# Optimization experiments

Measured on AMD Instinct MI355X. Metric: run time of the kernel, lower is better.

## Reference

```python
import jax, jax.numpy as jnp
import numpy as np
import math

HIDDEN_DIM = 1024
NUM_HEADS = 16
HEAD_DIM = HIDDEN_DIM // NUM_HEADS  # 64

def setup_inputs() -> dict:
    key = jax.random.key(0)
    k1, k2, k3 = jax.random.split(key, 3)
    x = jax.random.normal(k1, (8, 4096, HIDDEN_DIM), dtype=jnp.float32)
    W = jax.random.normal(k2, (HIDDEN_DIM, NUM_HEADS), dtype=jnp.float32) * (1.0 / math.sqrt(HIDDEN_DIM))
    mask = jax.random.randint(k3, (8, 4096), 0, 2, dtype=jnp.int32)
    return {"x": x, "W": W, "mask": mask}

def reference(x, W, mask):
    B, S, D = x.shape
    # linear scoring: [B,S,H], scaled by sqrt(head_dim)
    logits = jnp.einsum('bsd,dh->bsh', x, W) / math.sqrt(HEAD_DIM)
    # mask out padded positions (mask==0 -> -inf) before softmax over seq axis
    logits = jnp.where(mask[:, :, None] == 0, -jnp.inf, logits)
    attn = jax.nn.softmax(logits, axis=1)  # softmax over sequence dim
    # dropout is identity in eval mode
    # weighted sum: original expands x over heads, so each head pools the full hidden vector
    pooled = jnp.einsum('bsh,bsd->bhd', attn, x)  # [B, H, D]
    return pooled.reshape(B, NUM_HEADS * D)
```

## Files before the change

### kernel.cpp

```cpp
#include <hip/hip_runtime.h>
#include <math.h>

#define BB 8
#define SS 4096
#define DD 1024
#define HH 16

typedef __attribute__((ext_vector_type(4))) float f32x4;
typedef __fp16 fp16x2 __attribute__((ext_vector_type(2)));
typedef _Float16 half8v __attribute__((ext_vector_type(8)));


__device__ __forceinline__ void sm_merge(float& m, float& z, float om, float oz) {
  float nm = fmaxf(m, om);
  if (nm > -INFINITY)
    z = z * __expf(m - nm) + oz * __expf(om - nm);
  m = nm;
}

__global__ __launch_bounds__(256) void k_prepw(
    const float* __restrict__ W, ushort* __restrict__ wh16, ushort* __restrict__ wl16) {
  int i = blockIdx.x * 256 + threadIdx.x;
  int t = i >> 9;
  int l = (i >> 3) & 63;
  int e = i & 7;
  int d = t * 32 + (l >> 4) * 8 + e;
  int h = l & 15;
  float w = W[d * HH + h];
  _Float16 wh = (_Float16)w;
  _Float16 wl = (_Float16)(w - (float)wh);
  union { _Float16 f; ushort u; } ch, cl;
  ch.f = wh; cl.f = wl;
  wh16[i] = ch.u;
  wl16[i] = cl.u;
}

#define XLOAD(dst, c)                                                          \
  _Pragma("unroll") for (int k = 0; k < 4; ++k) {                              \
    int row = k * 4 + srow;                                                    \
    dst[k] = *reinterpret_cast<const float4*>(                                 \
        xw + (size_t)row * DD + (c) * 64 + sul * 4);                           \
  }
#define XSTAGE(src, c)                                                         \
  _Pragma("unroll") for (int k = 0; k < 4; ++k) {                              \
    int row = k * 4 + srow;                                                    \
    lds4[(c) & 1][wv][row][sul ^ (row & 7)] = src[k];                          \
  }
#define WLOAD(c)                                                               \
  whf[(c) & 1][0] = bhp[(2 * (c) + 0) * 64];                                   \
  whf[(c) & 1][1] = bhp[(2 * (c) + 1) * 64];                                   \
  wlf[(c) & 1][0] = blp[(2 * (c) + 0) * 64];                                   \
  wlf[(c) & 1][1] = blp[(2 * (c) + 1) * 64];

__global__ __launch_bounds__(256, 2) void k_logits(
    const float* __restrict__ x, const ushort* __restrict__ wh16,
    const ushort* __restrict__ wl16, const int* __restrict__ mask,
    float* __restrict__ plog, float2* __restrict__ bred) {
  __shared__ float4 lds4[2][4][16][16];
  __shared__ float2 smch[4][16];

  const int tid = threadIdx.x;
  const int lane = tid & 63;
  const int wv = __builtin_amdgcn_readfirstlane(tid >> 6);
  const int b = blockIdx.x >> 6;
  const int tile = blockIdx.x & 63;
  const int s0 = tile * 64;
  const int r15 = lane & 15;
  const int kg = lane >> 4;
  const int srow = lane >> 4;
  const int sul = lane & 15;

  const float* xw = x + ((size_t)b * SS + s0 + wv * 16) * DD;
  const half8v* bhp = reinterpret_cast<const half8v*>(wh16) + lane;
  const half8v* blp = reinterpret_cast<const half8v*>(wl16) + lane;

  f32x4 acch = {0.f, 0.f, 0.f, 0.f};
  f32x4 accl = {0.f, 0.f, 0.f, 0.f};
  float4 st[3][4];
  half8v whf[2][2], wlf[2][2];

  XLOAD(st[0], 0);
  XLOAD(st[1], 1);
  XLOAD(st[2], 2);
  XSTAGE(st[0], 0);
  WLOAD(0);
  WLOAD(1);

#pragma unroll
  for (int c = 0; c < 16; ++c) {
    if (c < 13) { XLOAD(st[(c + 3) % 3], c + 3); }

#pragma unroll
    for (int t4 = 0; t4 < 2; ++t4) {
      const int u0 = t4 * 8 + kg * 2;
      float4 va = lds4[c & 1][wv][r15][u0 ^ (r15 & 7)];
      float4 vb = lds4[c & 1][wv][r15][(u0 + 1) ^ (r15 & 7)];
      union { fp16x2 h2[4]; half8v h8; } ax;
      ax.h2[0] = __builtin_amdgcn_cvt_pkrtz(va.x, va.y);
      ax.h2[1] = __builtin_amdgcn_cvt_pkrtz(va.z, va.w);
      ax.h2[2] = __builtin_amdgcn_cvt_pkrtz(vb.x, vb.y);
      ax.h2[3] = __builtin_amdgcn_cvt_pkrtz(vb.z, vb.w);
      acch = __builtin_amdgcn_mfma_f32_16x16x32_f16(ax.h8, whf[c & 1][t4], acch, 0, 0, 0);
      accl = __builtin_amdgcn_mfma_f32_16x16x32_f16(ax.h8, wlf[c & 1][t4], accl, 0, 0, 0);
    }

    if (c < 14) { WLOAD(c + 2); }
    if (c < 15) { XSTAGE(st[(c + 1) % 3], c + 1); }
  }

  float lv[4];
  float* ob = plog + ((size_t)b * SS + s0 + wv * 16) * HH;
#pragma unroll
  for (int q = 0; q < 4; ++q) {
    int srw = kg * 4 + q;
    int msk = mask[b * SS + s0 + wv * 16 + srw];
    float v = (acch[q] + accl[q]) * 0.125f;
    lv[q] = msk ? v : -INFINITY;
    ob[(size_t)srw * HH + r15] = lv[q];
  }
  float ml = fmaxf(fmaxf(lv[0], lv[1]), fmaxf(lv[2], lv[3]));
  float zl = 0.f;
  if (ml > -INFINITY) {
#pragma unroll
    for (int q = 0; q < 4; ++q) zl += __expf(lv[q] - ml);
  }
#pragma unroll
  for (int off = 16; off < 64; off <<= 1) {
    float om = __shfl_xor(ml, off, 64);
    float oz = __shfl_xor(zl, off, 64);
    sm_merge(ml, zl, om, oz);
  }
  if (kg == 0) smch[wv][r15] = make_float2(ml, zl);
  __syncthreads();
  if (tid < 16) {
    float2 p0 = smch[0][tid];
    float m = p0.x, z = p0.y;
#pragma unroll
    for (int w = 1; w < 4; ++w) {
      float2 pw = smch[w][tid];
      sm_merge(m, z, pw.x, pw.y);
    }
    bred[((size_t)b * 64 + tile) * HH + tid] = make_float2(m, z);
  }
}

__global__ __launch_bounds__(256) void k_pool(
    const float* __restrict__ x, const float* __restrict__ plog,
    const float2* __restrict__ bred, const int* __restrict__ mask,
    float* __restrict__ partial) {
  __shared__ float wl[128][16];
  __shared__ float fm[16], fz[16];
  const int tid = threadIdx.x;
  const int dh = blockIdx.x & 1;
  const int sc = (blockIdx.x >> 1) & 31;
  const int b = blockIdx.x >> 6;
  const int s0 = sc * 128;

  if (tid < 16) {
    float m = -INFINITY, z = 0.f;
#pragma unroll 4
    for (int c = 0; c < 64; ++c) {
      float2 p = bred[((size_t)b * 64 + c) * HH + tid];
      sm_merge(m, z, p.x, p.y);
    }
    fm[tid] = m;
    fz[tid] = (z > 0.f) ? 1.0f / z : 0.f;
  }
  __syncthreads();

  const float4* p0 = reinterpret_cast<const float4*>(plog + ((size_t)b * SS + s0) * HH);
  const int* mb = mask + b * SS + s0;
#pragma unroll
  for (int k = 0; k < 2; ++k) {
    int f = k * 256 + tid;
    float4 va = p0[f];
    int msk = mb[f >> 2];
    int hb = (f & 3) * 4;
    float4 w;
    w.x = msk ? __expf(va.x - fm[hb + 0]) * fz[hb + 0] : 0.f;
    w.y = msk ? __expf(va.y - fm[hb + 1]) * fz[hb + 1] : 0.f;
    w.z = msk ? __expf(va.z - fm[hb + 2]) * fz[hb + 2] : 0.f;
    w.w = msk ? __expf(va.w - fm[hb + 3]) * fz[hb + 3] : 0.f;
    *reinterpret_cast<float4*>(&wl[0][0] + f * 4) = w;
  }
  __syncthreads();

  float2 acc[HH];
#pragma unroll
  for (int h = 0; h < HH; ++h) acc[h] = make_float2(0.f, 0.f);

  const float* xb = x + ((size_t)b * SS + s0) * DD + dh * 512 + tid * 2;
  for (int s = 0; s < 128; ++s) {
    float2 xv = *reinterpret_cast<const float2*>(xb + (size_t)s * DD);
    const float4* wrow = reinterpret_cast<const float4*>(wl[s]);
    float4 wa = wrow[0], wb_ = wrow[1], wc = wrow[2], wd = wrow[3];
    float wvv[16] = {wa.x, wa.y, wa.z, wa.w, wb_.x, wb_.y, wb_.z, wb_.w,
                     wc.x, wc.y, wc.z, wc.w, wd.x, wd.y, wd.z, wd.w};
#pragma unroll
    for (int h = 0; h < HH; ++h) {
      float w = wvv[h];
      acc[h].x += w * xv.x;
      acc[h].y += w * xv.y;
    }
  }

  float* pb = partial + ((size_t)sc * BB + b) * (HH * DD) + dh * 512 + tid * 2;
#pragma unroll
  for (int h = 0; h < HH; ++h)
    *reinterpret_cast<float2*>(pb + (size_t)h * DD) = acc[h];
}

__global__ __launch_bounds__(256) void k_reduce(
    const float* __restrict__ partial, float* __restrict__ out) {
  const int idx = blockIdx.x * 256 + threadIdx.x;
  float s = 0.f;
#pragma unroll
  for (int c = 0; c < 32; ++c) s += partial[(size_t)c * (BB * HH * DD) + idx];
  out[idx] = s;
}

extern "C" void kernel_launch(void* const* d_in, const int* in_sizes, int n_in,
                              void* d_out, int out_size, void* d_ws, size_t ws_size,
                              hipStream_t stream) {
  const float* x = (const float*)d_in[0];
  const float* W = (const float*)d_in[1];
  const int* mask = (const int*)d_in[2];
  float* out = (float*)d_out;

  char* ws = (char*)d_ws;
  float* plog    = (float*)ws;
  float* partial = (float*)(ws + (size_t)6 * 1024 * 1024);
  ushort* wh16   = (ushort*)(ws + (size_t)22 * 1024 * 1024);
  ushort* wl16   = (ushort*)(ws + (size_t)22 * 1024 * 1024 + 32 * 1024);
  float2* bred   = (float2*)(ws + (size_t)23 * 1024 * 1024);

  k_prepw<<<64, 256, 0, stream>>>(W, wh16, wl16);
  k_logits<<<512, 256, 0, stream>>>(x, wh16, wl16, mask, plog, bred);
  k_pool<<<512, 256, 0, stream>>>(x, plog, bred, mask, partial);
  k_reduce<<<512, 256, 0, stream>>>(partial, out);
}
```

Measured before the change: 70.99 us.

## Drop split-fp16 weight correction and pool from fp16 copy of x

Removes the low-part fp16 weight term, so logits are computed with a single fp16 MFMA instead of a hi/lo pair. The logits kernel also writes an fp16 copy of x into workspace, and the pooling kernel reads that copy instead of fp32 x. This halves the bytes the second pass over x reads, at the cost of an extra fp16 write. It lowers accuracy for both the logits and the pooled output, which may break tolerance.

After: 84.13 us. +18.5%, slower.

```diff
diff --git a/kernel.cpp b/kernel.cpp
--- a/kernel.cpp
+++ b/kernel.cpp
@@ -19,20 +19,16 @@
 }
 
 __global__ __launch_bounds__(256) void k_prepw(
-    const float* __restrict__ W, ushort* __restrict__ wh16, ushort* __restrict__ wl16) {
+    const float* __restrict__ W, ushort* __restrict__ wh16) {
   int i = blockIdx.x * 256 + threadIdx.x;
   int t = i >> 9;
   int l = (i >> 3) & 63;
   int e = i & 7;
   int d = t * 32 + (l >> 4) * 8 + e;
   int h = l & 15;
-  float w = W[d * HH + h];
-  _Float16 wh = (_Float16)w;
-  _Float16 wl = (_Float16)(w - (float)wh);
-  union { _Float16 f; ushort u; } ch, cl;
-  ch.f = wh; cl.f = wl;
-  wh16[i] = ch.u;
-  wl16[i] = cl.u;
+  union { _Float16 f; ushort u; } cv;
+  cv.f = (_Float16)W[d * HH + h];
+  wh16[i] = cv.u;
 }
 
 #define XLOAD(dst, c)                                                          \
@@ -48,14 +44,12 @@
   }
 #define WLOAD(c)                                                               \
   whf[(c) & 1][0] = bhp[(2 * (c) + 0) * 64];                                   \
-  whf[(c) & 1][1] = bhp[(2 * (c) + 1) * 64];                                   \
-  wlf[(c) & 1][0] = blp[(2 * (c) + 0) * 64];                                   \
-  wlf[(c) & 1][1] = blp[(2 * (c) + 1) * 64];
+  whf[(c) & 1][1] = bhp[(2 * (c) + 1) * 64];
 
 __global__ __launch_bounds__(256, 2) void k_logits(
     const float* __restrict__ x, const ushort* __restrict__ wh16,
-    const ushort* __restrict__ wl16, const int* __restrict__ mask,
-    float* __restrict__ plog, float2* __restrict__ bred) {
+    const int* __restrict__ mask, float* __restrict__ plog,
+    float2* __restrict__ bred, ushort* __restrict__ xh) {
   __shared__ float4 lds4[2][4][16][16];
   __shared__ float2 smch[4][16];
 
@@ -72,12 +66,11 @@
 
   const float* xw = x + ((size_t)b * SS + s0 + wv * 16) * DD;
   const half8v* bhp = reinterpret_cast<const half8v*>(wh16) + lane;
-  const half8v* blp = reinterpret_cast<const half8v*>(wl16) + lane;
+  ushort* xhw = xh + ((size_t)b * SS + s0 + wv * 16 + r15) * DD + kg * 8;
 
   f32x4 acch = {0.f, 0.f, 0.f, 0.f};
-  f32x4 accl = {0.f, 0.f, 0.f, 0.f};
   float4 st[3][4];
-  half8v whf[2][2], wlf[2][2];
+  half8v whf[2][2];
 
   XLOAD(st[0], 0);
   XLOAD(st[1], 1);
@@ -101,7 +94,7 @@
       ax.h2[2] = __builtin_amdgcn_cvt_pkrtz(vb.x, vb.y);
       ax.h2[3] = __builtin_amdgcn_cvt_pkrtz(vb.z, vb.w);
       acch = __builtin_amdgcn_mfma_f32_16x16x32_f16(ax.h8, whf[c & 1][t4], acch, 0, 0, 0);
-      accl = __builtin_amdgcn_mfma_f32_16x16x32_f16(ax.h8, wlf[c & 1][t4], accl, 0, 0, 0);
+      *reinterpret_cast<half8v*>(xhw + (size_t)c * 64 + t4 * 32) = ax.h8;
     }
 
     if (c < 14) { WLOAD(c + 2); }
@@ -114,7 +107,7 @@
   for (int q = 0; q < 4; ++q) {
     int srw = kg * 4 + q;
     int msk = mask[b * SS + s0 + wv * 16 + srw];
-    float v = (acch[q] + accl[q]) * 0.125f;
+    float v = acch[q] * 0.125f;
     lv[q] = msk ? v : -INFINITY;
     ob[(size_t)srw * HH + r15] = lv[q];
   }
@@ -145,7 +138,7 @@
 }
 
 __global__ __launch_bounds__(256) void k_pool(
-    const float* __restrict__ x, const float* __restrict__ plog,
+    const ushort* __restrict__ xh, const float* __restrict__ plog,
     const float2* __restrict__ bred, const int* __restrict__ mask,
     float* __restrict__ partial) {
   __shared__ float wl[128][16];
@@ -189,9 +182,10 @@
 #pragma unroll
   for (int h = 0; h < HH; ++h) acc[h] = make_float2(0.f, 0.f);
 
-  const float* xb = x + ((size_t)b * SS + s0) * DD + dh * 512 + tid * 2;
+  const ushort* xb = xh + ((size_t)b * SS + s0) * DD + dh * 512 + tid * 2;
   for (int s = 0; s < 128; ++s) {
-    float2 xv = *reinterpret_cast<const float2*>(xb + (size_t)s * DD);
+    fp16x2 xv2 = *reinterpret_cast<const fp16x2*>(xb + (size_t)s * DD);
+    float xvx = (float)xv2.x, xvy = (float)xv2.y;
     const float4* wrow = reinterpret_cast<const float4*>(wl[s]);
     float4 wa = wrow[0], wb_ = wrow[1], wc = wrow[2], wd = wrow[3];
     float wvv[16] = {wa.x, wa.y, wa.z, wa.w, wb_.x, wb_.y, wb_.z, wb_.w,
@@ -199,8 +193,8 @@
 #pragma unroll
     for (int h = 0; h < HH; ++h) {
       float w = wvv[h];
-      acc[h].x += w * xv.x;
-      acc[h].y += w * xv.y;
+      acc[h].x += w * xvx;
+      acc[h].y += w * xvy;
     }
   }
 
@@ -231,11 +225,11 @@
   float* plog    = (float*)ws;
   float* partial = (float*)(ws + (size_t)6 * 1024 * 1024);
   ushort* wh16   = (ushort*)(ws + (size_t)22 * 1024 * 1024);
-  ushort* wl16   = (ushort*)(ws + (size_t)22 * 1024 * 1024 + 32 * 1024);
   float2* bred   = (float2*)(ws + (size_t)23 * 1024 * 1024);
-
-  k_prepw<<<64, 256, 0, stream>>>(W, wh16, wl16);
-  k_logits<<<512, 256, 0, stream>>>(x, wh16, wl16, mask, plog, bred);
-  k_pool<<<512, 256, 0, stream>>>(x, plog, bred, mask, partial);
+  ushort* xh     = (ushort*)(ws + (size_t)24 * 1024 * 1024);
+
+  k_prepw<<<64, 256, 0, stream>>>(W, wh16);
+  k_logits<<<512, 256, 0, stream>>>(x, wh16, mask, plog, bred, xh);
+  k_pool<<<512, 256, 0, stream>>>(xh, plog, bred, mask, partial);
   k_reduce<<<512, 256, 0, stream>>>(partial, out);
 }
```

## Fuse pooling and cross-chunk reduction by splitting pool work over hidden columns

Applied to the files above, without the earlier changes.

Replaces the sequence-chunked pooling kernel plus separate reduction kernel with a single kernel where each block owns 16 hidden columns across the full sequence and reduces per-thread partial sums in shared memory. This removes the partial-sum buffer round trip through global memory and one kernel launch. In exchange, x is read in narrow 64-byte row segments with large strides, and softmax weights are recomputed by every block for the whole sequence.

Result: slower. 103.2 us (+45.4%).

```diff
diff --git a/kernel.cpp b/kernel.cpp
--- a/kernel.cpp
+++ b/kernel.cpp
@@ -144,17 +144,18 @@
   }
 }
 
-__global__ __launch_bounds__(256) void k_pool(
+__global__ __launch_bounds__(256) void k_pool2(
     const float* __restrict__ x, const float* __restrict__ plog,
     const float2* __restrict__ bred, const int* __restrict__ mask,
-    float* __restrict__ partial) {
-  __shared__ float wl[128][16];
+    float* __restrict__ out) {
+  __shared__ float wl[256][16];
+  __shared__ float red[16][16][17];
   __shared__ float fm[16], fz[16];
   const int tid = threadIdx.x;
-  const int dh = blockIdx.x & 1;
-  const int sc = (blockIdx.x >> 1) & 31;
+  const int spar = tid >> 4;
+  const int dlane = tid & 15;
   const int b = blockIdx.x >> 6;
-  const int s0 = sc * 128;
+  const int dsl = blockIdx.x & 63;
 
   if (tid < 16) {
     float m = -INFINITY, z = 0.f;
@@ -168,55 +169,54 @@
   }
   __syncthreads();
 
-  const float4* p0 = reinterpret_cast<const float4*>(plog + ((size_t)b * SS + s0) * HH);
-  const int* mb = mask + b * SS + s0;
-#pragma unroll
-  for (int k = 0; k < 2; ++k) {
-    int f = k * 256 + tid;
-    float4 va = p0[f];
-    int msk = mb[f >> 2];
-    int hb = (f & 3) * 4;
-    float4 w;
-    w.x = msk ? __expf(va.x - fm[hb + 0]) * fz[hb + 0] : 0.f;
-    w.y = msk ? __expf(va.y - fm[hb + 1]) * fz[hb + 1] : 0.f;
-    w.z = msk ? __expf(va.z - fm[hb + 2]) * fz[hb + 2] : 0.f;
-    w.w = msk ? __expf(va.w - fm[hb + 3]) * fz[hb + 3] : 0.f;
-    *reinterpret_cast<float4*>(&wl[0][0] + f * 4) = w;
-  }
+  float acc[HH];
+#pragma unroll
+  for (int h = 0; h < HH; ++h) acc[h] = 0.f;
+
+  const float4* p0 = reinterpret_cast<const float4*>(plog + (size_t)b * SS * HH);
+  const int* mb = mask + b * SS;
+  const float* xb = x + (size_t)b * SS * DD + dsl * 16 + dlane;
+
+  for (int cs = 0; cs < 16; ++cs) {
+    __syncthreads();
+#pragma unroll
+    for (int k = 0; k < 4; ++k) {
+      int f = k * 256 + tid;
+      float4 va = p0[cs * 1024 + f];
+      int msk = mb[cs * 256 + (f >> 2)];
+      int hb = (f & 3) * 4;
+      float4 w;
+      w.x = msk ? __expf(va.x - fm[hb + 0]) * fz[hb + 0] : 0.f;
+      w.y = msk ? __expf(va.y - fm[hb + 1]) * fz[hb + 1] : 0.f;
+      w.z = msk ? __expf(va.z - fm[hb + 2]) * fz[hb + 2] : 0.f;
+      w.w = msk ? __expf(va.w - fm[hb + 3]) * fz[hb + 3] : 0.f;
+      *reinterpret_cast<float4*>(&wl[0][0] + f * 4) = w;
+    }
+    __syncthreads();
+
+#pragma unroll 4
+    for (int si = 0; si < 256; si += 16) {
+      int s = si + spar;
+      float xv = xb[(size_t)(cs * 256 + s) * DD];
+      const float4* wrow = reinterpret_cast<const float4*>(wl[s]);
+      float4 wa = wrow[0], wb_ = wrow[1], wc = wrow[2], wd = wrow[3];
+      float wvv[16] = {wa.x, wa.y, wa.z, wa.w, wb_.x, wb_.y, wb_.z, wb_.w,
+                       wc.x, wc.y, wc.z, wc.w, wd.x, wd.y, wd.z, wd.w};
+#pragma unroll
+      for (int h = 0; h < HH; ++h) acc[h] += wvv[h] * xv;
+    }
+  }
+
+#pragma unroll
+  for (int h = 0; h < HH; ++h) red[spar][h][dlane] = acc[h];
   __syncthreads();
-
-  float2 acc[HH];
-#pragma unroll
-  for (int h = 0; h < HH; ++h) acc[h] = make_float2(0.f, 0.f);
-
-  const float* xb = x + ((size_t)b * SS + s0) * DD + dh * 512 + tid * 2;
-  for (int s = 0; s < 128; ++s) {
-    float2 xv = *reinterpret_cast<const float2*>(xb + (size_t)s * DD);
-    const float4* wrow = reinterpret_cast<const float4*>(wl[s]);
-    float4 wa = wrow[0], wb_ = wrow[1], wc = wrow[2], wd = wrow[3];
-    float wvv[16] = {wa.x, wa.y, wa.z, wa.w, wb_.x, wb_.y, wb_.z, wb_.w,
-                     wc.x, wc.y, wc.z, wc.w, wd.x, wd.y, wd.z, wd.w};
-#pragma unroll
-    for (int h = 0; h < HH; ++h) {
-      float w = wvv[h];
-      acc[h].x += w * xv.x;
-      acc[h].y += w * xv.y;
-    }
-  }
-
-  float* pb = partial + ((size_t)sc * BB + b) * (HH * DD) + dh * 512 + tid * 2;
-#pragma unroll
-  for (int h = 0; h < HH; ++h)
-    *reinterpret_cast<float2*>(pb + (size_t)h * DD) = acc[h];
-}
-
-__global__ __launch_bounds__(256) void k_reduce(
-    const float* __restrict__ partial, float* __restrict__ out) {
-  const int idx = blockIdx.x * 256 + threadIdx.x;
-  float s = 0.f;
-#pragma unroll
-  for (int c = 0; c < 32; ++c) s += partial[(size_t)c * (BB * HH * DD) + idx];
-  out[idx] = s;
+  {
+    const int h = tid >> 4, dl = tid & 15;
+    float s = 0.f;
+#pragma unroll
+    for (int p = 0; p < 16; ++p) s += red[p][h][dl];
+    out[(size_t)b * (HH * DD) + h * DD + dsl * 16 + dl] = s;
+  }
 }
 
 extern "C" void kernel_launch(void* const* d_in, const int* in_sizes, int n_in,
@@ -229,13 +229,11 @@
 
   char* ws = (char*)d_ws;
   float* plog    = (float*)ws;
-  float* partial = (float*)(ws + (size_t)6 * 1024 * 1024);
   ushort* wh16   = (ushort*)(ws + (size_t)22 * 1024 * 1024);
   ushort* wl16   = (ushort*)(ws + (size_t)22 * 1024 * 1024 + 32 * 1024);
   float2* bred   = (float2*)(ws + (size_t)23 * 1024 * 1024);
 
   k_prepw<<<64, 256, 0, stream>>>(W, wh16, wl16);
   k_logits<<<512, 256, 0, stream>>>(x, wh16, wl16, mask, plog, bred);
-  k_pool<<<512, 256, 0, stream>>>(x, plog, bred, mask, partial);
-  k_reduce<<<512, 256, 0, stream>>>(partial, out);
-}
+  k_pool2<<<512, 256, 0, stream>>>(x, plog, bred, mask, out);
+}
```
